# Kernel tuning notes

Hardware: AMD Instinct MI355X
Metric: run time of the kernel (lower is better)

Reference implementation:

```python
import jax, jax.numpy as jnp
import numpy as np

B, T, S0 = 8, 4, 4096
D_MODEL, H, D, R, RANK = 2048, 16, 128, 64, 512
C = D - R  # content dim = 64


def _rope(x, positions):
    # x: [B, H, T, R]; rotate-half style RoPE as in the torch module
    half = x.shape[-1] // 2
    inv_freq = 1.0 / (10000.0 ** (jnp.arange(half, dtype=jnp.float32) / half))
    freqs = positions.astype(jnp.float32)[:, None] * inv_freq[None, :]  # [T, half]
    cos = jnp.cos(freqs)[None, None].astype(x.dtype)
    sin = jnp.sin(freqs)[None, None].astype(x.dtype)
    x1, x2 = x[..., :half], x[..., half:]
    return jnp.concatenate([x1 * cos - x2 * sin, x1 * sin + x2 * cos], axis=-1)


def setup_inputs() -> dict:
    key = jax.random.key(0)
    ks = jax.random.split(key, 9)
    s = 0.02
    return {
        "x": jax.random.normal(ks[0], (B, T, D_MODEL), jnp.float32),
        "cache_c_kv": jax.random.normal(ks[1], (B, S0, RANK), jnp.float32),
        "cache_k_rope": jax.random.normal(ks[2], (B, S0, H, R), jnp.float32),
        "w_q": jax.random.normal(ks[3], (D_MODEL, H * C), jnp.float32) * s,
        "w_q_rope": jax.random.normal(ks[4], (D_MODEL, H * R), jnp.float32) * s,
        "w_kv_down": jax.random.normal(ks[5], (D_MODEL, RANK), jnp.float32) * s,
        "w_kv_up": jax.random.normal(ks[6], (RANK, H * D), jnp.float32) * s,
        "w_k_rope": jax.random.normal(ks[7], (D_MODEL, H * R), jnp.float32) * s,
        "w_out": jax.random.normal(ks[8], (H * D, D_MODEL), jnp.float32) * s,
    }


def reference(x, cache_c_kv, cache_k_rope, w_q, w_q_rope, w_kv_down, w_kv_up, w_k_rope, w_out):
    cache_len = cache_c_kv.shape[1]
    positions = jnp.arange(cache_len, cache_len + T)

    # queries
    q_content = (x @ w_q).reshape(B, T, H, C).transpose(0, 2, 1, 3)        # [B,H,T,C]
    q_rope = (x @ w_q_rope).reshape(B, T, H, R).transpose(0, 2, 1, 3)      # [B,H,T,R]
    q_rope = _rope(q_rope, positions)
    q = jnp.concatenate([q_content, q_rope], axis=-1)                       # [B,H,T,D]

    # new compressed kv + rope keys, append to cache
    c_kv_new = x @ w_kv_down                                                # [B,T,RANK]
    k_rope_new = (x @ w_k_rope).reshape(B, T, H, R).transpose(0, 2, 1, 3)
    k_rope_new = _rope(k_rope_new, positions).transpose(0, 2, 1, 3)         # [B,T,H,R]
    c_kv = jnp.concatenate([cache_c_kv, c_kv_new], axis=1)                  # [B,S,RANK]
    k_rope = jnp.concatenate([cache_k_rope, k_rope_new], axis=1)            # [B,S,H,R]

    # decompress full cache every step (the expensive MLA pattern)
    S = c_kv.shape[1]
    kv = (c_kv @ w_kv_up).reshape(B, S, H, D)                               # [B,S,H,D]
    k_content = kv[..., :C].transpose(0, 2, 1, 3)                           # [B,H,S,C]
    v = kv.transpose(0, 2, 1, 3)                                            # [B,H,S,D]
    k = jnp.concatenate([k_content, k_rope.transpose(0, 2, 1, 3)], axis=-1) # [B,H,S,D]

    # kv_cache present => is_prefill False => no causal mask (faithful to source)
    scale = 1.0 / jnp.sqrt(jnp.asarray(D, dtype=q.dtype))
    scores = jnp.einsum('bhtd,bhsd->bhts', q, k) * scale
    attn = jax.nn.softmax(scores, axis=-1)
    out = jnp.einsum('bhts,bhsd->bhtd', attn, v)                            # [B,H,T,D]
    out = out.transpose(0, 2, 1, 3).reshape(B, T, H * D)
    return out @ w_out                                                       # [B,T,D_MODEL]
```

## Files before the change

kernel.cpp:

```cpp
#include <hip/hip_runtime.h>
#include <cmath>

#define BB 8
#define TT 4
#define HH 16
#define DDIM 128
#define RRDIM 64
#define CCDIM 64
#define RANKC 512
#define DMODEL 2048
#define S0C 4096
#define NQ 64
#define HD 2048
#define NACT 3584
#define NSC 65
#define SCC 64
#define SCALE_ATT 0.08838834764831845f

#define AIDX(row, kk) ((row)*132 + (((row)>>2)<<2) + (kk))

__global__ __launch_bounds__(256) void k_proj4(const float* __restrict__ A,
                                               const float* __restrict__ w0,
                                               const float* __restrict__ w1,
                                               const float* __restrict__ w2,
                                               const float* __restrict__ w3,
                                               float* __restrict__ part) {
  __shared__ float a_lds[4352];
  const int tid = threadIdx.x;
  const int cb = blockIdx.x;
  const int k0 = blockIdx.y * 128;
  const float* W; int N, lc0, off;
  if (cb < 8)       { W = w0; N = 1024; lc0 = cb * 128;        off = 0; }
  else if (cb < 16) { W = w1; N = 1024; lc0 = (cb - 8) * 128;  off = 1024; }
  else if (cb < 20) { W = w2; N = 512;  lc0 = (cb - 16) * 128; off = 2048; }
  else              { W = w3; N = 1024; lc0 = (cb - 20) * 128; off = 2560; }
  {
    const int row = tid >> 3;
    const int kseg = (tid & 7) * 16;
    const float4* s4 = reinterpret_cast<const float4*>(A + (size_t)row * DMODEL + k0 + kseg);
    float4 v0 = s4[0], v1 = s4[1], v2 = s4[2], v3 = s4[3];
    *reinterpret_cast<float4*>(&a_lds[AIDX(row, kseg)])      = v0;
    *reinterpret_cast<float4*>(&a_lds[AIDX(row, kseg + 4)])  = v1;
    *reinterpret_cast<float4*>(&a_lds[AIDX(row, kseg + 8)])  = v2;
    *reinterpret_cast<float4*>(&a_lds[AIDX(row, kseg + 12)]) = v3;
  }
  __syncthreads();
  const int cg = tid & 31;
  const int rg = tid >> 5;
  float acc[4][4];
  #pragma unroll
  for (int r = 0; r < 4; ++r)
    #pragma unroll
    for (int c = 0; c < 4; ++c) acc[r][c] = 0.f;
  #pragma unroll 4
  for (int kk = 0; kk < 128; ++kk) {
    const float4 w4 = *reinterpret_cast<const float4*>(W + (size_t)(k0 + kk) * N + lc0 + cg * 4);
    const float wv[4] = {w4.x, w4.y, w4.z, w4.w};
    #pragma unroll
    for (int r = 0; r < 4; ++r) {
      const float av = a_lds[AIDX(rg * 4 + r, kk)];
      #pragma unroll
      for (int c = 0; c < 4; ++c) acc[r][c] = fmaf(av, wv[c], acc[r][c]);
    }
  }
  #pragma unroll
  for (int r = 0; r < 4; ++r) {
    float4 o = make_float4(acc[r][0], acc[r][1], acc[r][2], acc[r][3]);
    *reinterpret_cast<float4*>(part + ((size_t)blockIdx.y * 32 + rg * 4 + r) * NACT + off + lc0 + cg * 4) = o;
  }
}

__global__ __launch_bounds__(256) void k_proj(const float* __restrict__ A,
                                              const float* __restrict__ W,
                                              float* __restrict__ part,
                                              int N, int NTOT, int coloff) {
  __shared__ float a_lds[4352];
  const int tid = threadIdx.x;
  const int c0 = blockIdx.x * 128;
  const int k0 = blockIdx.y * 128;
  {
    const int row = tid >> 3;
    const int kseg = (tid & 7) * 16;
    const float4* s4 = reinterpret_cast<const float4*>(A + (size_t)row * DMODEL + k0 + kseg);
    float4 v0 = s4[0], v1 = s4[1], v2 = s4[2], v3 = s4[3];
    *reinterpret_cast<float4*>(&a_lds[AIDX(row, kseg)])      = v0;
    *reinterpret_cast<float4*>(&a_lds[AIDX(row, kseg + 4)])  = v1;
    *reinterpret_cast<float4*>(&a_lds[AIDX(row, kseg + 8)])  = v2;
    *reinterpret_cast<float4*>(&a_lds[AIDX(row, kseg + 12)]) = v3;
  }
  __syncthreads();
  const int cg = tid & 31;
  const int rg = tid >> 5;
  float acc[4][4];
  #pragma unroll
  for (int r = 0; r < 4; ++r)
    #pragma unroll
    for (int c = 0; c < 4; ++c) acc[r][c] = 0.f;
  #pragma unroll 4
  for (int kk = 0; kk < 128; ++kk) {
    const float4 w4 = *reinterpret_cast<const float4*>(W + (size_t)(k0 + kk) * N + c0 + cg * 4);
    const float wv[4] = {w4.x, w4.y, w4.z, w4.w};
    #pragma unroll
    for (int r = 0; r < 4; ++r) {
      const float av = a_lds[AIDX(rg * 4 + r, kk)];
      #pragma unroll
      for (int c = 0; c < 4; ++c) acc[r][c] = fmaf(av, wv[c], acc[r][c]);
    }
  }
  #pragma unroll
  for (int r = 0; r < 4; ++r) {
    float4 o = make_float4(acc[r][0], acc[r][1], acc[r][2], acc[r][3]);
    *reinterpret_cast<float4*>(part + ((size_t)blockIdx.y * 32 + rg * 4 + r) * NTOT + coloff + c0 + cg * 4) = o;
  }
}

__global__ __launch_bounds__(256) void k_reduce(const float* __restrict__ part,
                                                float* __restrict__ out, int total, int nsplit) {
  int g = blockIdx.x * 256 + threadIdx.x;
  if (g >= total) return;
  float s = 0.f;
  #pragma unroll 4
  for (int c = 0; c < nsplit; ++c) s += part[(size_t)c * total + g];
  out[g] = s;
}

__global__ __launch_bounds__(256) void k_qlatrope(const float* __restrict__ act,
                                                  const float* __restrict__ wup,
                                                  float* __restrict__ qlat,
                                                  float* __restrict__ qrope,
                                                  float* __restrict__ ckvn,
                                                  float* __restrict__ krn) {
  __shared__ float wt[64 * 132];
  __shared__ float a_s[32 * 68];
  const int tid = threadIdx.x;
  const int bx = blockIdx.x;
  if (bx < 64) {
    const int h = bx & 15;
    const int r0 = (bx >> 4) * 128;
    {
      const int r = tid >> 1;
      const int cseg = (tid & 1) * 32;
      const float* src = wup + (size_t)(r0 + r) * HD + h * DDIM + cseg;
      #pragma unroll
      for (int u = 0; u < 8; ++u) {
        const float4 v = *reinterpret_cast<const float4*>(src + u * 4);
        wt[(cseg + u * 4 + 0) * 132 + r] = v.x;
        wt[(cseg + u * 4 + 1) * 132 + r] = v.y;
        wt[(cseg + u * 4 + 2) * 132 + r] = v.z;
        wt[(cseg + u * 4 + 3) * 132 + r] = v.w;
      }
    }
    {
      const int bt = tid >> 3;
      const int cseg = (tid & 7) * 8;
      const float4* s4 = reinterpret_cast<const float4*>(act + (size_t)bt * NACT + h * CCDIM + cseg);
      float4 v0 = s4[0], v1 = s4[1];
      *reinterpret_cast<float4*>(&a_s[bt * 68 + cseg])     = v0;
      *reinterpret_cast<float4*>(&a_s[bt * 68 + cseg + 4]) = v1;
    }
    __syncthreads();
    const int r = tid & 127;
    const int bth = tid >> 7;
    float acc[16];
    #pragma unroll
    for (int i = 0; i < 16; ++i) acc[i] = 0.f;
    #pragma unroll 8
    for (int c = 0; c < 64; ++c) {
      const float wv = wt[c * 132 + r];
      #pragma unroll
      for (int i = 0; i < 16; ++i)
        acc[i] = fmaf(a_s[(bth * 16 + i) * 68 + c], wv, acc[i]);
    }
    #pragma unroll
    for (int i = 0; i < 16; ++i) {
      const int bt = bth * 16 + i;
      const int b = bt >> 2, t = bt & 3;
      qlat[((size_t)(b * NQ) + h * TT + t) * RANKC + r0 + r] = acc[i];
    }
    return;
  }
  int g = (bx - 64) * 256 + tid;
  if (g < BB * TT * HH * 32) {
    const int hj = g & 31;
    const int h = (g >> 5) & 15;
    const int t = (g >> 9) & 3;
    const int b = g >> 11;
    const float* arow = act + (size_t)(b * TT + t) * NACT + 1024 + h * RRDIM;
    const float x1 = arow[hj], x2 = arow[hj + 32];
    const double fr = (double)(S0C + t) * pow(10000.0, -(double)hj / 32.0);
    const float cs = (float)cos(fr), sn = (float)sin(fr);
    const int qi = h * TT + t;
    qrope[((size_t)b * NQ + qi) * RRDIM + hj]      = x1 * cs - x2 * sn;
    qrope[((size_t)b * NQ + qi) * RRDIM + hj + 32] = x1 * sn + x2 * cs;
    return;
  }
  g -= BB * TT * HH * 32;
  if (g < BB * TT * HH * 32) {
    const int hj = g & 31;
    const int h = (g >> 5) & 15;
    const int t = (g >> 9) & 3;
    const int b = g >> 11;
    const float* arow = act + (size_t)(b * TT + t) * NACT + 2560 + h * RRDIM;
    const float x1 = arow[hj], x2 = arow[hj + 32];
    const double fr = (double)(S0C + t) * pow(10000.0, -(double)hj / 32.0);
    const float cs = (float)cos(fr), sn = (float)sin(fr);
    krn[((size_t)(b * TT + t) * HH + h) * RRDIM + hj]      = x1 * cs - x2 * sn;
    krn[((size_t)(b * TT + t) * HH + h) * RRDIM + hj + 32] = x1 * sn + x2 * cs;
    return;
  }
  g -= BB * TT * HH * 32;
  if (g < BB * TT * RANKC) {
    ckvn[g] = act[(size_t)(g >> 9) * NACT + 2048 + (g & 511)];
  }
}

__global__ __launch_bounds__(256) void k_attn(
    const float* __restrict__ cache_ckv, const float* __restrict__ cache_kr,
    const float* __restrict__ ckvn, const float* __restrict__ krn,
    const float* __restrict__ qlat, const float* __restrict__ qrope,
    float* __restrict__ ml, float* __restrict__ olat) {
  __shared__ float sm[13056];
  float* const A0  = sm;
  float* const Bt0 = sm + 2176;
  float* const A1  = sm + 4352;
  float* const Bt1 = sm + 6528;
  float* const p_t = sm + 8704;
  float* const qr_l = sm;
  float* const CS0 = sm;
  float* const CS1 = sm + 4352;

  const int tid = threadIdx.x;
  const int ty = tid >> 4, tx = tid & 15;
  const int b = blockIdx.x, chunk = blockIdx.y;
  int scnt;
  const float *ckv, *kr;
  if (chunk < 64) {
    scnt = SCC;
    ckv = cache_ckv + ((size_t)b * S0C + (size_t)chunk * SCC) * RANKC;
    kr  = cache_kr  + ((size_t)b * S0C + (size_t)chunk * SCC) * (HH * RRDIM);
  } else {
    scnt = TT;
    ckv = ckvn + (size_t)b * TT * RANKC;
    kr  = krn  + (size_t)b * TT * (HH * RRDIM);
  }
  const float* qlb = qlat + (size_t)b * NQ * RANKC;
  const float* qrb = qrope + (size_t)b * NQ * RRDIM;

  {
    const int row = tid >> 2;
    const int seg = (tid & 3) * 16;
    const float4* s4 = reinterpret_cast<const float4*>(qrb + (size_t)row * RRDIM + seg);
    float4 v0 = s4[0], v1 = s4[1], v2 = s4[2], v3 = s4[3];
    float4* d4 = reinterpret_cast<float4*>(&qr_l[row * 68 + seg]);
    d4[0] = v0; d4[1] = v1; d4[2] = v2; d4[3] = v3;
  }
  __syncthreads();
  {
    const int l = tx;
    for (int it = 0; it < scnt; ++it) {
      const float4 kv = *reinterpret_cast<const float4*>(kr + (size_t)(it * HH + ty) * RRDIM + l * 4);
      float p0, p1, p2, p3;
      {
        const float4 q0 = *reinterpret_cast<const float4*>(&qr_l[(ty * 4 + 0) * 68 + l * 4]);
        const float4 q1 = *reinterpret_cast<const float4*>(&qr_l[(ty * 4 + 1) * 68 + l * 4]);
        const float4 q2 = *reinterpret_cast<const float4*>(&qr_l[(ty * 4 + 2) * 68 + l * 4]);
        const float4 q3 = *reinterpret_cast<const float4*>(&qr_l[(ty * 4 + 3) * 68 + l * 4]);
        p0 = kv.x*q0.x + kv.y*q0.y + kv.z*q0.z + kv.w*q0.w;
        p1 = kv.x*q1.x + kv.y*q1.y + kv.z*q1.z + kv.w*q1.w;
        p2 = kv.x*q2.x + kv.y*q2.y + kv.z*q2.z + kv.w*q2.w;
        p3 = kv.x*q3.x + kv.y*q3.y + kv.z*q3.z + kv.w*q3.w;
      }
      #pragma unroll
      for (int off = 1; off < 16; off <<= 1) {
        p0 += __shfl_xor(p0, off, 16);
        p1 += __shfl_xor(p1, off, 16);
        p2 += __shfl_xor(p2, off, 16);
        p3 += __shfl_xor(p3, off, 16);
      }
      if (l < 4) {
        const float v = (l == 0) ? p0 : (l == 1) ? p1 : (l == 2) ? p2 : p3;
        p_t[it * 68 + ty * 4 + l] = v;
      }
    }
  }
  __syncthreads();

  float acc[4][4];
  #pragma unroll
  for (int i = 0; i < 4; ++i)
    #pragma unroll
    for (int j = 0; j < 4; ++j)
      acc[i][j] = p_t[(tx * 4 + j) * 68 + ty * 4 + i];

  auto stageAB = [&](int kc, float* aDst, float* bDst) {
    const int row = tid >> 2;
    const int kb = (tid & 3) * 8;
    {
      const float4* s4 = reinterpret_cast<const float4*>(qlb + (size_t)row * RANKC + kc + kb);
      float4 v0 = s4[0], v1 = s4[1];
      aDst[(kb+0)*68+row]=v0.x; aDst[(kb+1)*68+row]=v0.y; aDst[(kb+2)*68+row]=v0.z; aDst[(kb+3)*68+row]=v0.w;
      aDst[(kb+4)*68+row]=v1.x; aDst[(kb+5)*68+row]=v1.y; aDst[(kb+6)*68+row]=v1.z; aDst[(kb+7)*68+row]=v1.w;
    }
    {
      float4 v0, v1;
      if (row < scnt) {
        const float4* s4 = reinterpret_cast<const float4*>(ckv + (size_t)row * RANKC + kc + kb);
        v0 = s4[0]; v1 = s4[1];
      } else { v0 = make_float4(0.f,0.f,0.f,0.f); v1 = v0; }
      bDst[(kb+0)*68+row]=v0.x; bDst[(kb+1)*68+row]=v0.y; bDst[(kb+2)*68+row]=v0.z; bDst[(kb+3)*68+row]=v0.w;
      bDst[(kb+4)*68+row]=v1.x; bDst[(kb+5)*68+row]=v1.y; bDst[(kb+6)*68+row]=v1.z; bDst[(kb+7)*68+row]=v1.w;
    }
  };
  stageAB(0, A0, Bt0);
  __syncthreads();
  for (int kt = 0; kt < 16; ++kt) {
    const float* aCur = (kt & 1) ? A1 : A0;
    const float* bCur = (kt & 1) ? Bt1 : Bt0;
    if (kt < 15) stageAB((kt + 1) * 32, (kt & 1) ? A0 : A1, (kt & 1) ? Bt0 : Bt1);
    #pragma unroll 8
    for (int kk = 0; kk < 32; ++kk) {
      const float4 av = *reinterpret_cast<const float4*>(&aCur[kk * 68 + ty * 4]);
      const float4 bv = *reinterpret_cast<const float4*>(&bCur[kk * 68 + tx * 4]);
      const float a_[4] = {av.x, av.y, av.z, av.w};
      const float b_[4] = {bv.x, bv.y, bv.z, bv.w};
      #pragma unroll
      for (int i = 0; i < 4; ++i)
        #pragma unroll
        for (int j = 0; j < 4; ++j)
          acc[i][j] = fmaf(a_[i], b_[j], acc[i][j]);
    }
    __syncthreads();
  }

  #pragma unroll
  for (int i = 0; i < 4; ++i) {
    float mx = -1e30f;
    #pragma unroll
    for (int j = 0; j < 4; ++j) {
      const int s = tx * 4 + j;
      float v = (s < scnt) ? acc[i][j] * SCALE_ATT : -1e30f;
      acc[i][j] = v;
      mx = fmaxf(mx, v);
    }
    #pragma unroll
    for (int off = 1; off < 16; off <<= 1) mx = fmaxf(mx, __shfl_xor(mx, off, 16));
    float sum = 0.f;
    #pragma unroll
    for (int j = 0; j < 4; ++j) {
      const float p = __expf(acc[i][j] - mx);
      acc[i][j] = p;
      sum += p;
    }
    #pragma unroll
    for (int off = 1; off < 16; off <<= 1) sum += __shfl_xor(sum, off, 16);
    #pragma unroll
    for (int j = 0; j < 4; ++j)
      p_t[(tx * 4 + j) * 68 + ty * 4 + i] = acc[i][j];
    if (tx == 0) {
      const size_t mb = (((size_t)b * NSC + chunk) * NQ + ty * 4 + i) * 2;
      ml[mb] = mx; ml[mb + 1] = sum;
    }
  }

  auto stageCS = [&](int step, float* dst) {
    const int rq = step >> 1, sck = step & 1;
    const int s_loc = tid >> 3;
    const int c16 = (tid & 7) * 16;
    const int s = sck * 32 + s_loc;
    float4 v[4];
    if (s < scnt) {
      const float4* s4 = reinterpret_cast<const float4*>(ckv + (size_t)s * RANKC + rq * 128 + c16);
      v[0]=s4[0]; v[1]=s4[1]; v[2]=s4[2]; v[3]=s4[3];
    } else { v[0]=make_float4(0.f,0.f,0.f,0.f); v[1]=v[0]; v[2]=v[0]; v[3]=v[0]; }
    float4* d4 = reinterpret_cast<float4*>(&dst[s_loc * 136 + c16]);
    d4[0]=v[0]; d4[1]=v[1]; d4[2]=v[2]; d4[3]=v[3];
  };
  stageCS(0, CS0);
  __syncthreads();
  const size_t obase = ((size_t)b * NSC + chunk) * NQ * RANKC;
  float acc2[4][8];
  for (int step = 0; step < 8; ++step) {
    const float* cs = (step & 1) ? CS1 : CS0;
    if (step < 7) stageCS(step + 1, (step & 1) ? CS0 : CS1);
    const int rq = step >> 1, sck = step & 1;
    if (sck == 0) {
      #pragma unroll
      for (int i = 0; i < 4; ++i)
        #pragma unroll
        for (int j = 0; j < 8; ++j) acc2[i][j] = 0.f;
    }
    #pragma unroll 8
    for (int ss = 0; ss < 32; ++ss) {
      const int s = sck * 32 + ss;
      const float4 pv = *reinterpret_cast<const float4*>(&p_t[s * 68 + ty * 4]);
      const float4 c0 = *reinterpret_cast<const float4*>(&cs[ss * 136 + tx * 4]);
      const float4 c1 = *reinterpret_cast<const float4*>(&cs[ss * 136 + 64 + tx * 4]);
      const float p_[4] = {pv.x, pv.y, pv.z, pv.w};
      const float cv[8] = {c0.x, c0.y, c0.z, c0.w, c1.x, c1.y, c1.z, c1.w};
      #pragma unroll
      for (int i = 0; i < 4; ++i)
        #pragma unroll
        for (int j = 0; j < 8; ++j)
          acc2[i][j] = fmaf(p_[i], cv[j], acc2[i][j]);
    }
    if (sck == 1) {
      #pragma unroll
      for (int i = 0; i < 4; ++i) {
        const size_t rbase = obase + (size_t)(ty * 4 + i) * RANKC + rq * 128;
        *reinterpret_cast<float4*>(&olat[rbase + tx * 4])      = make_float4(acc2[i][0], acc2[i][1], acc2[i][2], acc2[i][3]);
        *reinterpret_cast<float4*>(&olat[rbase + 64 + tx * 4]) = make_float4(acc2[i][4], acc2[i][5], acc2[i][6], acc2[i][7]);
      }
    }
    __syncthreads();
  }
}

__global__ __launch_bounds__(512) void k_combF(const float* __restrict__ ml,
                                               const float* __restrict__ olat,
                                               const float* __restrict__ wup,
                                               float* __restrict__ ohead) {
  __shared__ float wrow[4][66];
  __shared__ float att_lds[4][516];
  const int h = blockIdx.x, b = blockIdx.y;
  const int tid = threadIdx.x;
  const int wave = tid >> 6;
  const int i = wave >> 1;
  const int rhalf = wave & 1;
  const int rl = tid & 63;
  const int qi = h * TT + i;
  float m1 = -1e30f, l1 = 0.f, m2 = -1e30f, l2 = 0.f;
  {
    const size_t base = (((size_t)b * NSC + rl) * NQ + qi) * 2;
    m1 = ml[base]; l1 = ml[base + 1];
    if (rl == 0) {
      const size_t b2 = (((size_t)b * NSC + 64) * NQ + qi) * 2;
      m2 = ml[b2]; l2 = ml[b2 + 1];
    }
  }
  float M = fmaxf(m1, m2);
  #pragma unroll
  for (int off = 1; off < 64; off <<= 1) M = fmaxf(M, __shfl_xor(M, off));
  float L = l1 * __expf(m1 - M) + ((rl == 0) ? l2 * __expf(m2 - M) : 0.f);
  #pragma unroll
  for (int off = 1; off < 64; off <<= 1) L += __shfl_xor(L, off);
  const float invL = 1.0f / L;
  wrow[i][rl] = __expf(m1 - M) * invL;
  if (rl == 0) wrow[i][64] = __expf(m2 - M) * invL;
  __syncthreads();
  const int r0 = rhalf * 256 + rl * 4;
  float o0 = 0.f, o1 = 0.f, o2 = 0.f, o3 = 0.f;
  for (int c = 0; c < NSC; ++c) {
    const float w = wrow[i][c];
    const float4 v = *reinterpret_cast<const float4*>(olat + (((size_t)b * NSC + c) * NQ + qi) * RANKC + r0);
    o0 = fmaf(v.x, w, o0); o1 = fmaf(v.y, w, o1); o2 = fmaf(v.z, w, o2); o3 = fmaf(v.w, w, o3);
  }
  *reinterpret_cast<float4*>(&att_lds[i][r0]) = make_float4(o0, o1, o2, o3);
  __syncthreads();
  const int col = tid & 127;
  const int t = tid >> 7;
  float acc = 0.f;
  #pragma unroll 8
  for (int r = 0; r < RANKC; ++r)
    acc = fmaf(att_lds[t][r], wup[(size_t)r * HD + h * DDIM + col], acc);
  ohead[(size_t)(b * TT + t) * HD + h * DDIM + col] = acc;
}

extern "C" void kernel_launch(void* const* d_in, const int* in_sizes, int n_in,
                              void* d_out, int out_size, void* d_ws, size_t ws_size,
                              hipStream_t stream) {
  const float* x     = (const float*)d_in[0];
  const float* cckv  = (const float*)d_in[1];
  const float* ckr   = (const float*)d_in[2];
  const float* w_q   = (const float*)d_in[3];
  const float* w_qr  = (const float*)d_in[4];
  const float* w_kvd = (const float*)d_in[5];
  const float* w_kvu = (const float*)d_in[6];
  const float* w_kr  = (const float*)d_in[7];
  const float* w_out = (const float*)d_in[8];
  float* out = (float*)d_out;
  float* ws = (float*)d_ws;

  size_t off = 0;
  float* act   = ws + off; off += 32ull * NACT;
  float* qlat  = ws + off; off += (size_t)BB * NQ * RANKC;
  float* qrope = ws + off; off += (size_t)BB * NQ * RRDIM;
  float* ckvn  = ws + off; off += (size_t)BB * TT * RANKC;
  float* krn   = ws + off; off += (size_t)BB * TT * HH * RRDIM;
  float* mlb   = ws + off; off += (size_t)BB * NSC * NQ * 2;
  float* ohead = ws + off; off += 32ull * HD;
  float* regB  = ws + off;
  float* part0 = regB;
  float* olat  = regB;
  float* part3 = regB;

  k_proj4<<<dim3(28, 16), 256, 0, stream>>>(x, w_q, w_qr, w_kvd, w_kr, part0);
  k_reduce<<<dim3(448), 256, 0, stream>>>(part0, act, 32 * NACT, 16);
  k_qlatrope<<<dim3(256), 256, 0, stream>>>(act, w_kvu, qlat, qrope, ckvn, krn);

  k_attn<<<dim3(BB, NSC), 256, 0, stream>>>(cckv, ckr, ckvn, krn, qlat, qrope, mlb, olat);

  k_combF<<<dim3(16, 8), 512, 0, stream>>>(mlb, olat, w_kvu, ohead);
  k_proj<<<dim3(16, 16), 256, 0, stream>>>(ohead, w_out, part3, 2048, 2048, 0);
  k_reduce<<<dim3(256), 256, 0, stream>>>(part3, out, 32 * HD, 16);
}
```

Measured before the change: 230.6 us.

## Split rope scores into separate kernel, register-staged prefetch, bf16 partial outputs

Moves the rope-key score computation out of the attention kernel into a new k_rscore kernel spread over 1152 blocks, which writes per-head score rows that k_attn then loads as its initial accumulators. The global-to-LDS staging in k_attn now loads the next tile into registers before the compute loop and writes it to LDS afterwards, so load latency overlaps the FMAs. The per-chunk latent outputs are stored as bf16 and widened in k_combF, halving that intermediate's traffic at some precision cost. This adds one kernel launch and a 512x4160 fp32 score buffer round-trip.

```diff
diff --git a/kernel.cpp b/kernel.cpp
--- a/kernel.cpp
+++ b/kernel.cpp
@@ -14,10 +14,22 @@
 #define HD 2048
 #define NACT 3584
 #define NSC 65
-#define SCC 64
+#define SPAD 4160
 #define SCALE_ATT 0.08838834764831845f
 
 #define AIDX(row, kk) ((row)*132 + (((row)>>2)<<2) + (kk))
+
+static __device__ __forceinline__ unsigned short f2bf(float x) {
+  unsigned u = __float_as_uint(x);
+  u += 0x7FFFu + ((u >> 16) & 1u);
+  return (unsigned short)(u >> 16);
+}
+static __device__ __forceinline__ float bf2f(unsigned v16) {
+  return __uint_as_float(v16 << 16);
+}
+static __device__ __forceinline__ unsigned pk2(float a, float b) {
+  return (unsigned)f2bf(a) | ((unsigned)f2bf(b) << 16);
+}
 
 __global__ __launch_bounds__(256) void k_proj4(const float* __restrict__ A,
                                                const float* __restrict__ w0,
@@ -214,113 +226,110 @@
   }
 }
 
+__global__ __launch_bounds__(256) void k_rscore(const float* __restrict__ cache_kr,
+                                                const float* __restrict__ krn,
+                                                const float* __restrict__ qrope,
+                                                float* __restrict__ rs) {
+  const int bh = blockIdx.x;
+  const int b = bh >> 4, h = bh & 15;
+  const int tid = threadIdx.x;
+  const int ql = tid & 3;
+  float4 qf[4][4];
+  const float* qrb = qrope + ((size_t)b * NQ + h * TT) * RRDIM;
+  #pragma unroll
+  for (int t = 0; t < 4; ++t)
+    #pragma unroll
+    for (int u = 0; u < 4; ++u)
+      qf[t][u] = *reinterpret_cast<const float4*>(qrb + t * RRDIM + ql * 16 + u * 4);
+  const int s0 = blockIdx.y * 512;
+  #pragma unroll 1
+  for (int pass = 0; pass < 8; ++pass) {
+    const int s = s0 + pass * 64 + (tid >> 2);
+    if (s < 4100) {
+      const float* krow = (s < S0C)
+        ? cache_kr + (((size_t)b * S0C + s) * HH + h) * RRDIM
+        : krn + (((size_t)b * TT + (s - S0C)) * HH + h) * RRDIM;
+      float p[4] = {0.f, 0.f, 0.f, 0.f};
+      #pragma unroll
+      for (int u = 0; u < 4; ++u) {
+        const float4 kv = *reinterpret_cast<const float4*>(krow + ql * 16 + u * 4);
+        #pragma unroll
+        for (int t = 0; t < 4; ++t) {
+          p[t] += kv.x * qf[t][u].x + kv.y * qf[t][u].y
+                + kv.z * qf[t][u].z + kv.w * qf[t][u].w;
+        }
+      }
+      #pragma unroll
+      for (int t = 0; t < 4; ++t) {
+        p[t] += __shfl_xor(p[t], 1, 4);
+        p[t] += __shfl_xor(p[t], 2, 4);
+      }
+      rs[((size_t)bh * 4 + ql) * SPAD + s] = p[ql];
+    }
+  }
+}
+
 __global__ __launch_bounds__(256) void k_attn(
-    const float* __restrict__ cache_ckv, const float* __restrict__ cache_kr,
-    const float* __restrict__ ckvn, const float* __restrict__ krn,
-    const float* __restrict__ qlat, const float* __restrict__ qrope,
-    float* __restrict__ ml, float* __restrict__ olat) {
+    const float* __restrict__ cache_ckv, const float* __restrict__ ckvn,
+    const float* __restrict__ rs, const float* __restrict__ qlat,
+    float* __restrict__ ml, unsigned short* __restrict__ olat) {
   __shared__ float sm[13056];
-  float* const A0  = sm;
-  float* const Bt0 = sm + 2176;
-  float* const A1  = sm + 4352;
-  float* const Bt1 = sm + 6528;
+  float* const A0 = sm;
+  float* const A1 = sm + 2176;
+  float* const B0 = sm + 4352;
+  float* const B1 = sm + 6528;
   float* const p_t = sm + 8704;
-  float* const qr_l = sm;
   float* const CS0 = sm;
   float* const CS1 = sm + 4352;
 
   const int tid = threadIdx.x;
   const int ty = tid >> 4, tx = tid & 15;
   const int b = blockIdx.x, chunk = blockIdx.y;
-  int scnt;
-  const float *ckv, *kr;
-  if (chunk < 64) {
-    scnt = SCC;
-    ckv = cache_ckv + ((size_t)b * S0C + (size_t)chunk * SCC) * RANKC;
-    kr  = cache_kr  + ((size_t)b * S0C + (size_t)chunk * SCC) * (HH * RRDIM);
-  } else {
-    scnt = TT;
-    ckv = ckvn + (size_t)b * TT * RANKC;
-    kr  = krn  + (size_t)b * TT * (HH * RRDIM);
-  }
+  const int scnt = (chunk < 64) ? 64 : TT;
+  const float* ckv = (chunk < 64)
+      ? cache_ckv + ((size_t)b * S0C + (size_t)chunk * 64) * RANKC
+      : ckvn + (size_t)b * TT * RANKC;
   const float* qlb = qlat + (size_t)b * NQ * RANKC;
-  const float* qrb = qrope + (size_t)b * NQ * RRDIM;
-
+
+  float acc[4][4];
   {
-    const int row = tid >> 2;
-    const int seg = (tid & 3) * 16;
-    const float4* s4 = reinterpret_cast<const float4*>(qrb + (size_t)row * RRDIM + seg);
-    float4 v0 = s4[0], v1 = s4[1], v2 = s4[2], v3 = s4[3];
-    float4* d4 = reinterpret_cast<float4*>(&qr_l[row * 68 + seg]);
-    d4[0] = v0; d4[1] = v1; d4[2] = v2; d4[3] = v3;
-  }
-  __syncthreads();
-  {
-    const int l = tx;
-    for (int it = 0; it < scnt; ++it) {
-      const float4 kv = *reinterpret_cast<const float4*>(kr + (size_t)(it * HH + ty) * RRDIM + l * 4);
-      float p0, p1, p2, p3;
-      {
-        const float4 q0 = *reinterpret_cast<const float4*>(&qr_l[(ty * 4 + 0) * 68 + l * 4]);
-        const float4 q1 = *reinterpret_cast<const float4*>(&qr_l[(ty * 4 + 1) * 68 + l * 4]);
-        const float4 q2 = *reinterpret_cast<const float4*>(&qr_l[(ty * 4 + 2) * 68 + l * 4]);
-        const float4 q3 = *reinterpret_cast<const float4*>(&qr_l[(ty * 4 + 3) * 68 + l * 4]);
-        p0 = kv.x*q0.x + kv.y*q0.y + kv.z*q0.z + kv.w*q0.w;
-        p1 = kv.x*q1.x + kv.y*q1.y + kv.z*q1.z + kv.w*q1.w;
-        p2 = kv.x*q2.x + kv.y*q2.y + kv.z*q2.z + kv.w*q2.w;
-        p3 = kv.x*q3.x + kv.y*q3.y + kv.z*q3.z + kv.w*q3.w;
-      }
-      #pragma unroll
-      for (int off = 1; off < 16; off <<= 1) {
-        p0 += __shfl_xor(p0, off, 16);
-        p1 += __shfl_xor(p1, off, 16);
-        p2 += __shfl_xor(p2, off, 16);
-        p3 += __shfl_xor(p3, off, 16);
-      }
-      if (l < 4) {
-        const float v = (l == 0) ? p0 : (l == 1) ? p1 : (l == 2) ? p2 : p3;
-        p_t[it * 68 + ty * 4 + l] = v;
-      }
-    }
-  }
-  __syncthreads();
-
-  float acc[4][4];
-  #pragma unroll
-  for (int i = 0; i < 4; ++i)
-    #pragma unroll
-    for (int j = 0; j < 4; ++j)
-      acc[i][j] = p_t[(tx * 4 + j) * 68 + ty * 4 + i];
-
-  auto stageAB = [&](int kc, float* aDst, float* bDst) {
-    const int row = tid >> 2;
-    const int kb = (tid & 3) * 8;
-    {
-      const float4* s4 = reinterpret_cast<const float4*>(qlb + (size_t)row * RANKC + kc + kb);
-      float4 v0 = s4[0], v1 = s4[1];
-      aDst[(kb+0)*68+row]=v0.x; aDst[(kb+1)*68+row]=v0.y; aDst[(kb+2)*68+row]=v0.z; aDst[(kb+3)*68+row]=v0.w;
-      aDst[(kb+4)*68+row]=v1.x; aDst[(kb+5)*68+row]=v1.y; aDst[(kb+6)*68+row]=v1.z; aDst[(kb+7)*68+row]=v1.w;
-    }
-    {
-      float4 v0, v1;
-      if (row < scnt) {
-        const float4* s4 = reinterpret_cast<const float4*>(ckv + (size_t)row * RANKC + kc + kb);
-        v0 = s4[0]; v1 = s4[1];
-      } else { v0 = make_float4(0.f,0.f,0.f,0.f); v1 = v0; }
-      bDst[(kb+0)*68+row]=v0.x; bDst[(kb+1)*68+row]=v0.y; bDst[(kb+2)*68+row]=v0.z; bDst[(kb+3)*68+row]=v0.w;
-      bDst[(kb+4)*68+row]=v1.x; bDst[(kb+5)*68+row]=v1.y; bDst[(kb+6)*68+row]=v1.z; bDst[(kb+7)*68+row]=v1.w;
-    }
+    const int sg = chunk * 64 + tx * 4;
+    #pragma unroll
+    for (int i = 0; i < 4; ++i) {
+      const float4 v = *reinterpret_cast<const float4*>(
+          rs + (((size_t)(b * HH + ty)) * 4 + i) * SPAD + sg);
+      acc[i][0] = v.x; acc[i][1] = v.y; acc[i][2] = v.z; acc[i][3] = v.w;
+    }
+  }
+
+  const int row = tid >> 2;
+  const int kb = (tid & 3) * 8;
+  float4 ra0, ra1, rb0, rb1;
+  auto loadAB = [&](int kc) {
+    const float4* a4 = reinterpret_cast<const float4*>(qlb + (size_t)row * RANKC + kc + kb);
+    ra0 = a4[0]; ra1 = a4[1];
+    if (row < scnt) {
+      const float4* b4 = reinterpret_cast<const float4*>(ckv + (size_t)row * RANKC + kc + kb);
+      rb0 = b4[0]; rb1 = b4[1];
+    } else { rb0 = make_float4(0.f, 0.f, 0.f, 0.f); rb1 = rb0; }
   };
-  stageAB(0, A0, Bt0);
+  auto writeAB = [&](float* aD, float* bD) {
+    aD[(kb+0)*68+row]=ra0.x; aD[(kb+1)*68+row]=ra0.y; aD[(kb+2)*68+row]=ra0.z; aD[(kb+3)*68+row]=ra0.w;
+    aD[(kb+4)*68+row]=ra1.x; aD[(kb+5)*68+row]=ra1.y; aD[(kb+6)*68+row]=ra1.z; aD[(kb+7)*68+row]=ra1.w;
+    bD[(kb+0)*68+row]=rb0.x; bD[(kb+1)*68+row]=rb0.y; bD[(kb+2)*68+row]=rb0.z; bD[(kb+3)*68+row]=rb0.w;
+    bD[(kb+4)*68+row]=rb1.x; bD[(kb+5)*68+row]=rb1.y; bD[(kb+6)*68+row]=rb1.z; bD[(kb+7)*68+row]=rb1.w;
+  };
+  loadAB(0);
+  writeAB(A0, B0);
   __syncthreads();
   for (int kt = 0; kt < 16; ++kt) {
-    const float* aCur = (kt & 1) ? A1 : A0;
-    const float* bCur = (kt & 1) ? Bt1 : Bt0;
-    if (kt < 15) stageAB((kt + 1) * 32, (kt & 1) ? A0 : A1, (kt & 1) ? Bt0 : Bt1);
+    if (kt < 15) loadAB((kt + 1) * 32);
+    const float* aC = (kt & 1) ? A1 : A0;
+    const float* bC = (kt & 1) ? B1 : B0;
     #pragma unroll 8
     for (int kk = 0; kk < 32; ++kk) {
-      const float4 av = *reinterpret_cast<const float4*>(&aCur[kk * 68 + ty * 4]);
-      const float4 bv = *reinterpret_cast<const float4*>(&bCur[kk * 68 + tx * 4]);
+      const float4 av = *reinterpret_cast<const float4*>(&aC[kk * 68 + ty * 4]);
+      const float4 bv = *reinterpret_cast<const float4*>(&bC[kk * 68 + tx * 4]);
       const float a_[4] = {av.x, av.y, av.z, av.w};
       const float b_[4] = {bv.x, bv.y, bv.z, bv.w};
       #pragma unroll
@@ -329,6 +338,7 @@
         for (int j = 0; j < 4; ++j)
           acc[i][j] = fmaf(a_[i], b_[j], acc[i][j]);
     }
+    if (kt < 15) writeAB((kt & 1) ? A0 : A1, (kt & 1) ? B0 : B1);
     __syncthreads();
   }
 
@@ -362,26 +372,29 @@
     }
   }
 
-  auto stageCS = [&](int step, float* dst) {
+  const int sl = tid >> 3;
+  const int c16 = (tid & 7) * 16;
+  float4 rc0, rc1, rc2, rc3;
+  auto loadC = [&](int step) {
     const int rq = step >> 1, sck = step & 1;
-    const int s_loc = tid >> 3;
-    const int c16 = (tid & 7) * 16;
-    const int s = sck * 32 + s_loc;
-    float4 v[4];
+    const int s = sck * 32 + sl;
     if (s < scnt) {
       const float4* s4 = reinterpret_cast<const float4*>(ckv + (size_t)s * RANKC + rq * 128 + c16);
-      v[0]=s4[0]; v[1]=s4[1]; v[2]=s4[2]; v[3]=s4[3];
-    } else { v[0]=make_float4(0.f,0.f,0.f,0.f); v[1]=v[0]; v[2]=v[0]; v[3]=v[0]; }
-    float4* d4 = reinterpret_cast<float4*>(&dst[s_loc * 136 + c16]);
-    d4[0]=v[0]; d4[1]=v[1]; d4[2]=v[2]; d4[3]=v[3];
+      rc0 = s4[0]; rc1 = s4[1]; rc2 = s4[2]; rc3 = s4[3];
+    } else { rc0 = make_float4(0.f, 0.f, 0.f, 0.f); rc1 = rc0; rc2 = rc0; rc3 = rc0; }
   };
-  stageCS(0, CS0);
+  auto writeC = [&](float* dst) {
+    float4* d4 = reinterpret_cast<float4*>(&dst[sl * 136 + c16]);
+    d4[0] = rc0; d4[1] = rc1; d4[2] = rc2; d4[3] = rc3;
+  };
+  loadC(0);
+  writeC(CS0);
   __syncthreads();
   const size_t obase = ((size_t)b * NSC + chunk) * NQ * RANKC;
   float acc2[4][8];
   for (int step = 0; step < 8; ++step) {
+    if (step < 7) loadC(step + 1);
     const float* cs = (step & 1) ? CS1 : CS0;
-    if (step < 7) stageCS(step + 1, (step & 1) ? CS0 : CS1);
     const int rq = step >> 1, sck = step & 1;
     if (sck == 0) {
       #pragma unroll
@@ -391,8 +404,7 @@
     }
     #pragma unroll 8
     for (int ss = 0; ss < 32; ++ss) {
-      const int s = sck * 32 + ss;
-      const float4 pv = *reinterpret_cast<const float4*>(&p_t[s * 68 + ty * 4]);
+      const float4 pv = *reinterpret_cast<const float4*>(&p_t[(sck * 32 + ss) * 68 + ty * 4]);
       const float4 c0 = *reinterpret_cast<const float4*>(&cs[ss * 136 + tx * 4]);
       const float4 c1 = *reinterpret_cast<const float4*>(&cs[ss * 136 + 64 + tx * 4]);
       const float p_[4] = {pv.x, pv.y, pv.z, pv.w};
@@ -403,12 +415,15 @@
         for (int j = 0; j < 8; ++j)
           acc2[i][j] = fmaf(p_[i], cv[j], acc2[i][j]);
     }
+    if (step < 7) writeC((step & 1) ? CS0 : CS1);
     if (sck == 1) {
       #pragma unroll
       for (int i = 0; i < 4; ++i) {
         const size_t rbase = obase + (size_t)(ty * 4 + i) * RANKC + rq * 128;
-        *reinterpret_cast<float4*>(&olat[rbase + tx * 4])      = make_float4(acc2[i][0], acc2[i][1], acc2[i][2], acc2[i][3]);
-        *reinterpret_cast<float4*>(&olat[rbase + 64 + tx * 4]) = make_float4(acc2[i][4], acc2[i][5], acc2[i][6], acc2[i][7]);
+        uint2 w0 = make_uint2(pk2(acc2[i][0], acc2[i][1]), pk2(acc2[i][2], acc2[i][3]));
+        uint2 w1 = make_uint2(pk2(acc2[i][4], acc2[i][5]), pk2(acc2[i][6], acc2[i][7]));
+        *reinterpret_cast<uint2*>(&olat[rbase + tx * 4])      = w0;
+        *reinterpret_cast<uint2*>(&olat[rbase + 64 + tx * 4]) = w1;
       }
     }
     __syncthreads();
@@ -416,7 +431,7 @@
 }
 
 __global__ __launch_bounds__(512) void k_combF(const float* __restrict__ ml,
-                                               const float* __restrict__ olat,
+                                               const unsigned short* __restrict__ olat,
                                                const float* __restrict__ wup,
                                                float* __restrict__ ohead) {
   __shared__ float wrow[4][66];
@@ -451,8 +466,12 @@
   float o0 = 0.f, o1 = 0.f, o2 = 0.f, o3 = 0.f;
   for (int c = 0; c < NSC; ++c) {
     const float w = wrow[i][c];
-    const float4 v = *reinterpret_cast<const float4*>(olat + (((size_t)b * NSC + c) * NQ + qi) * RANKC + r0);
-    o0 = fmaf(v.x, w, o0); o1 = fmaf(v.y, w, o1); o2 = fmaf(v.z, w, o2); o3 = fmaf(v.w, w, o3);
+    const uint2 v = *reinterpret_cast<const uint2*>(
+        olat + (((size_t)b * NSC + c) * NQ + qi) * RANKC + r0);
+    o0 = fmaf(bf2f(v.x & 0xffffu), w, o0);
+    o1 = fmaf(bf2f(v.x >> 16), w, o1);
+    o2 = fmaf(bf2f(v.y & 0xffffu), w, o2);
+    o3 = fmaf(bf2f(v.y >> 16), w, o3);
   }
   *reinterpret_cast<float4*>(&att_lds[i][r0]) = make_float4(o0, o1, o2, o3);
   __syncthreads();
@@ -488,16 +507,18 @@
   float* krn   = ws + off; off += (size_t)BB * TT * HH * RRDIM;
   float* mlb   = ws + off; off += (size_t)BB * NSC * NQ * 2;
   float* ohead = ws + off; off += 32ull * HD;
+  float* rsb   = ws + off; off += 512ull * SPAD;
   float* regB  = ws + off;
   float* part0 = regB;
-  float* olat  = regB;
+  unsigned short* olat = (unsigned short*)regB;
   float* part3 = regB;
 
   k_proj4<<<dim3(28, 16), 256, 0, stream>>>(x, w_q, w_qr, w_kvd, w_kr, part0);
   k_reduce<<<dim3(448), 256, 0, stream>>>(part0, act, 32 * NACT, 16);
   k_qlatrope<<<dim3(256), 256, 0, stream>>>(act, w_kvu, qlat, qrope, ckvn, krn);
-
-  k_attn<<<dim3(BB, NSC), 256, 0, stream>>>(cckv, ckr, ckvn, krn, qlat, qrope, mlb, olat);
+  k_rscore<<<dim3(128, 9), 256, 0, stream>>>(ckr, krn, qrope, rsb);
+
+  k_attn<<<dim3(BB, NSC), 256, 0, stream>>>(cckv, ckvn, rsb, qlat, mlb, olat);
 
   k_combF<<<dim3(16, 8), 512, 0, stream>>>(mlb, olat, w_kvu, ohead);
   k_proj<<<dim3(16, 16), 256, 0, stream>>>(ohead, w_out, part3, 2048, 2048, 0);
```

Measured after the change: 221.1 us. -4.1%, faster.
